# Kernel optimization log

Hardware: AMD Instinct MI355X
Metric: run time of the kernel (lower is better)

Reference implementation:

```python
import jax, jax.numpy as jnp
import numpy as np

B, S, D = 2, 4096, 1024
H, W = 16, 128
HD = D // H  # 64


def setup_inputs() -> dict:
    key = jax.random.key(0)
    ks = jax.random.split(key, 6)
    x = jax.random.normal(ks[0], (B, S, D), dtype=jnp.float32)
    # standard RoPE angle table: theta[pos, i] = pos / 10000^(2i/hd)
    inv_freq = 1.0 / (10000.0 ** (jnp.arange(0, HD, 2, dtype=jnp.float32) / HD))  # (hd/2,)
    rope_freqs = jnp.arange(S, dtype=jnp.float32)[:, None] * inv_freq[None, :]     # (S, hd/2)
    scale = 0.02
    wq = jax.random.normal(ks[1], (D, D), dtype=jnp.float32) * scale
    wk = jax.random.normal(ks[2], (D, D), dtype=jnp.float32) * scale
    wv = jax.random.normal(ks[3], (D, D), dtype=jnp.float32) * scale
    wo = jax.random.normal(ks[4], (D, D), dtype=jnp.float32) * scale
    return {"x": x, "rope_freqs": rope_freqs, "wq": wq, "wk": wk, "wv": wv, "wo": wo}


def reference(x, rope_freqs, wq, wk, wv, wo):
    Bsz, Sl, Dm = x.shape
    hd = Dm // H
    q = (x @ wq.T).reshape(Bsz, Sl, H, hd)
    k = (x @ wk.T).reshape(Bsz, Sl, H, hd)
    v = (x @ wv.T).reshape(Bsz, Sl, H, hd)

    # rotate-half RoPE, angles broadcast over batch and heads
    f = rope_freqs[:Sl]                               # (S, hd/2)
    cos = jnp.cos(f)[None, :, None, :]
    sin = jnp.sin(f)[None, :, None, :]

    def rope(t):
        t1, t2 = jnp.split(t, 2, axis=-1)
        return jnp.concatenate([t1 * cos - t2 * sin, t2 * cos + t1 * sin], axis=-1)

    q = rope(q)
    k = rope(k)

    # block-local sliding-window attention: window [q-left, q+right]
    Bk = W                       # block size == window size
    nb = Sl // Bk                # S assumed divisible by W
    left = W // 2
    right = W - left - 1

    pad = [(0, 0), (Bk, Bk), (0, 0), (0, 0)]
    kb = jnp.pad(k, pad).reshape(Bsz, nb + 2, Bk, H, hd)
    vb = jnp.pad(v, pad).reshape(Bsz, nb + 2, Bk, H, hd)
    # each query block attends to 3 consecutive key blocks (prev, self, next)
    k3 = jnp.concatenate([kb[:, :-2], kb[:, 1:-1], kb[:, 2:]], axis=2)  # (B,nb,3Bk,H,hd)
    v3 = jnp.concatenate([vb[:, :-2], vb[:, 1:-1], vb[:, 2:]], axis=2)
    qb = q.reshape(Bsz, nb, Bk, H, hd)

    scale = 1.0 / jnp.sqrt(jnp.asarray(hd, dtype=x.dtype))
    scores = jnp.einsum('bnqhd,bnkhd->bnhqk', qb, k3) * scale  # (B,nb,H,Bk,3Bk)

    r = jnp.arange(Bk)
    c = jnp.arange(3 * Bk)
    rel = c[None, :] - Bk - r[:, None]                  # key_pos - query_pos, (Bk,3Bk)
    win = (rel >= -left) & (rel <= right)
    blk = jnp.arange(nb)
    key_pos = blk[:, None] * Bk + c[None, :] - Bk       # (nb,3Bk) absolute key positions
    valid = (key_pos >= 0) & (key_pos < Sl)
    mask = win[None, :, :] & valid[:, None, :]          # (nb,Bk,3Bk)

    scores = jnp.where(mask[None, :, None, :, :], scores, jnp.asarray(-1e30, scores.dtype))
    probs = jax.nn.softmax(scores, axis=-1)
    out = jnp.einsum('bnhqk,bnkhd->bnqhd', probs, v3).reshape(Bsz, Sl, H * hd)
    return out @ wo.T
```

## Files before the change

### kernel.cpp

```cpp
#include <hip/hip_runtime.h>

typedef unsigned short u16;
typedef unsigned int   u32;
typedef __attribute__((ext_vector_type(4))) unsigned int u32x4;
typedef __attribute__((ext_vector_type(2))) unsigned int u32x2;
typedef __attribute__((ext_vector_type(8))) short        s16x8;
typedef __attribute__((ext_vector_type(4))) float        f32x4;
typedef __attribute__((ext_vector_type(2))) float        f32x2;

#define S_LEN 4096

typedef const __attribute__((address_space(1))) void gas_void;
typedef __attribute__((address_space(3))) void las_void;

__device__ __forceinline__ u16 f2bf(float f) {
    u32 u = __builtin_bit_cast(u32, f);
    u32 r = (u + 0x7fffu + ((u >> 16) & 1u)) >> 16;
    return (u16)r;
}
__device__ __forceinline__ float bflo(u32 w) { return __builtin_bit_cast(float, w << 16); }
__device__ __forceinline__ float bfhi(u32 w) { return __builtin_bit_cast(float, w & 0xffff0000u); }

__device__ __forceinline__ float rmax16(float v) {
    v = fmaxf(v, __shfl_xor(v, 1));
    v = fmaxf(v, __shfl_xor(v, 2));
    v = fmaxf(v, __shfl_xor(v, 4));
    v = fmaxf(v, __shfl_xor(v, 8));
    return v;
}
__device__ __forceinline__ float rsum16(float v) {
    v += __shfl_xor(v, 1);
    v += __shfl_xor(v, 2);
    v += __shfl_xor(v, 4);
    v += __shfl_xor(v, 8);
    return v;
}

__global__ __launch_bounds__(256)
void cvt_f32_bf16(const float* __restrict__ in, u16* __restrict__ out, int n4) {
    int i = blockIdx.x * 256 + threadIdx.x;
    if (i >= n4) return;
    const f32x4 v = *(const f32x4*)(in + (size_t)i * 4);
    u32x2 o;
    o.x = (u32)f2bf(v.x) | ((u32)f2bf(v.y) << 16);
    o.y = (u32)f2bf(v.z) | ((u32)f2bf(v.w) << 16);
    *(u32x2*)(out + (size_t)i * 4) = o;
}

__global__ __launch_bounds__(256)
void cvt_weights(const float* __restrict__ wq, const float* __restrict__ wk,
                 const float* __restrict__ wv, const float* __restrict__ wo,
                 u16* __restrict__ wqkv, u16* __restrict__ wob) {
    const int i   = blockIdx.x * 256 + threadIdx.x;
    const int sel = i >> 18;
    const int loc = i & 262143;
    const float* src = (sel == 0) ? wq : (sel == 1) ? wk : (sel == 2) ? wv : wo;
    u16* dst = (sel < 3) ? (wqkv + (size_t)sel * 1048576) : wob;
    const f32x4 v = *(const f32x4*)(src + (size_t)loc * 4);
    u32x2 o;
    o.x = (u32)f2bf(v.x) | ((u32)f2bf(v.y) << 16);
    o.y = (u32)f2bf(v.z) | ((u32)f2bf(v.w) << 16);
    *(u32x2*)(dst + (size_t)loc * 4) = o;
}

__global__ __launch_bounds__(256)
void rope_tab(const float* __restrict__ freqs, float* __restrict__ tab) {
    const int i = blockIdx.x * 256 + threadIdx.x;
    const float f = freqs[i];
    float sn, cs;
    sincosf(f, &sn, &cs);
    tab[i * 2]     = cs;
    tab[i * 2 + 1] = sn;
}

#define VMW0() asm volatile("s_waitcnt vmcnt(0)" ::: "memory")
#define LGKM0() do { asm volatile("s_waitcnt lgkmcnt(0)" ::: "memory"); \
                     __builtin_amdgcn_sched_barrier(0); } while (0)
#define DSR0(d, a)   asm volatile("ds_read_b128 %0, %1"              : "=v"(d) : "v"(a))
#define DSR(d, a, o) asm volatile("ds_read_b128 %0, %1 offset:" #o   : "=v"(d) : "v"(a))
#define MFMA16(a, b, c) __builtin_amdgcn_mfma_f32_16x16x32_bf16(a, b, c, 0, 0, 0)

#define FRAGS(P) s16x8 P##a0,P##a1,P##a2,P##a3,P##a4,P##a5,P##a6,P##a7, \
                       P##b0,P##b1,P##b2,P##b3,P##b4,P##b5,P##b6,P##b7

#define LOADTILE(P, CUR) do { \
    const u32 abase_ = ldsA + ((u32)(CUR) << 14) + arow; \
    const u32 bbase_ = ldsB + ((u32)(CUR) << 15) + brow; \
    const u32 aa0_ = abase_ + ck0, aa1_ = abase_ + ck1; \
    const u32 ba0_ = bbase_ + ck0, ba1_ = bbase_ + ck1; \
    DSR0(P##a0, aa0_); DSR(P##a1, aa0_, 2048); DSR(P##a2, aa0_, 4096); DSR(P##a3, aa0_, 6144); \
    DSR0(P##a4, aa1_); DSR(P##a5, aa1_, 2048); DSR(P##a6, aa1_, 4096); DSR(P##a7, aa1_, 6144); \
    DSR0(P##b0, ba0_); DSR(P##b1, ba0_, 2048); DSR(P##b2, ba0_, 4096); DSR(P##b3, ba0_, 6144); \
    DSR0(P##b4, ba1_); DSR(P##b5, ba1_, 2048); DSR(P##b6, ba1_, 4096); DSR(P##b7, ba1_, 6144); \
} while (0)

#define MFMA32(P) do { \
    __builtin_amdgcn_s_setprio(1); \
    acc[0][0]=MFMA16(P##a0,P##b0,acc[0][0]); acc[1][0]=MFMA16(P##a1,P##b0,acc[1][0]); \
    acc[2][0]=MFMA16(P##a2,P##b0,acc[2][0]); acc[3][0]=MFMA16(P##a3,P##b0,acc[3][0]); \
    acc[0][1]=MFMA16(P##a0,P##b1,acc[0][1]); acc[1][1]=MFMA16(P##a1,P##b1,acc[1][1]); \
    acc[2][1]=MFMA16(P##a2,P##b1,acc[2][1]); acc[3][1]=MFMA16(P##a3,P##b1,acc[3][1]); \
    acc[0][2]=MFMA16(P##a0,P##b2,acc[0][2]); acc[1][2]=MFMA16(P##a1,P##b2,acc[1][2]); \
    acc[2][2]=MFMA16(P##a2,P##b2,acc[2][2]); acc[3][2]=MFMA16(P##a3,P##b2,acc[3][2]); \
    acc[0][3]=MFMA16(P##a0,P##b3,acc[0][3]); acc[1][3]=MFMA16(P##a1,P##b3,acc[1][3]); \
    acc[2][3]=MFMA16(P##a2,P##b3,acc[2][3]); acc[3][3]=MFMA16(P##a3,P##b3,acc[3][3]); \
    acc[0][0]=MFMA16(P##a4,P##b4,acc[0][0]); acc[1][0]=MFMA16(P##a5,P##b4,acc[1][0]); \
    acc[2][0]=MFMA16(P##a6,P##b4,acc[2][0]); acc[3][0]=MFMA16(P##a7,P##b4,acc[3][0]); \
    acc[0][1]=MFMA16(P##a4,P##b5,acc[0][1]); acc[1][1]=MFMA16(P##a5,P##b5,acc[1][1]); \
    acc[2][1]=MFMA16(P##a6,P##b5,acc[2][1]); acc[3][1]=MFMA16(P##a7,P##b5,acc[3][1]); \
    acc[0][2]=MFMA16(P##a4,P##b6,acc[0][2]); acc[1][2]=MFMA16(P##a5,P##b6,acc[1][2]); \
    acc[2][2]=MFMA16(P##a6,P##b6,acc[2][2]); acc[3][2]=MFMA16(P##a7,P##b6,acc[3][2]); \
    acc[0][3]=MFMA16(P##a4,P##b7,acc[0][3]); acc[1][3]=MFMA16(P##a5,P##b7,acc[1][3]); \
    acc[2][3]=MFMA16(P##a6,P##b7,acc[2][3]); acc[3][3]=MFMA16(P##a7,P##b7,acc[3][3]); \
    __builtin_amdgcn_s_setprio(0); \
} while (0)

template<int MODE>
__global__ __launch_bounds__(512, 2)
void gemm_bt(const u16* __restrict__ A, const u16* __restrict__ Bw,
             void* __restrict__ Cv, const float* __restrict__ cstab) {
    __shared__ __align__(16) u16 As[2][8192];
    __shared__ __align__(16) u16 Bs[2][16384];
    const int t    = threadIdx.x;
    const int bm   = blockIdx.x << 7;
    const int bn   = blockIdx.y << 8;
    const int wave = t >> 6;
    const int wr   = (wave >> 2) & 1;
    const int wc   = wave & 3;
    const int lane = t & 63;
    const int fr   = lane & 15;
    const int kg   = lane >> 4;
    const int f7   = fr & 7;
    const int wq16 = wave << 9;
    const int K    = 1024;

    const int srow = t >> 3;
    const int cSw  = (t & 7) ^ (srow & 7);

    const u16* ga0 = A  + (size_t)(bm + srow) * K + (cSw << 3);
    const u16* ga1 = ga0 + (size_t)64 * K;
    const u16* gb0 = Bw + (size_t)(bn + srow) * K + (cSw << 3);
    const u16* gb1 = gb0 + (size_t)64 * K;
    const u16* gb2 = gb1 + (size_t)64 * K;
    const u16* gb3 = gb2 + (size_t)64 * K;

    f32x4 acc[4][4];
#pragma unroll
    for (int m = 0; m < 4; ++m)
#pragma unroll
        for (int n = 0; n < 4; ++n) acc[m][n] = f32x4{0.f, 0.f, 0.f, 0.f};

    FRAGS(X);
    FRAGS(Y);

#define STAGE(cur) do { \
    __builtin_amdgcn_global_load_lds((gas_void*)ga0, (las_void*)(&As[cur][wq16]),          16, 0, 0); \
    __builtin_amdgcn_global_load_lds((gas_void*)ga1, (las_void*)(&As[cur][4096 + wq16]),   16, 0, 0); \
    __builtin_amdgcn_global_load_lds((gas_void*)gb0, (las_void*)(&Bs[cur][wq16]),          16, 0, 0); \
    __builtin_amdgcn_global_load_lds((gas_void*)gb1, (las_void*)(&Bs[cur][4096 + wq16]),   16, 0, 0); \
    __builtin_amdgcn_global_load_lds((gas_void*)gb2, (las_void*)(&Bs[cur][8192 + wq16]),   16, 0, 0); \
    __builtin_amdgcn_global_load_lds((gas_void*)gb3, (las_void*)(&Bs[cur][12288 + wq16]),  16, 0, 0); \
    ga0 += 64; ga1 += 64; gb0 += 64; gb1 += 64; gb2 += 64; gb3 += 64; \
} while (0)

    const u32 ldsA = (u32)(size_t)(las_void*)&As[0][0];
    const u32 ldsB = (u32)(size_t)(las_void*)&Bs[0][0];
    const u32 arow = (u32)(((wr << 6) + fr) << 7);
    const u32 brow = (u32)(((wc << 6) + fr) << 7);
    const u32 ck0  = (u32)((kg ^ f7) << 4);
    const u32 ck1  = (u32)(((4 + kg) ^ f7) << 4);

    STAGE(0);
    VMW0();
    __builtin_amdgcn_s_barrier();
    LOADTILE(X, 0);
    STAGE(1);

#pragma unroll 1
    for (int j = 0; j < 16; j += 2) {
        LGKM0();
        VMW0();
        __builtin_amdgcn_s_barrier();
        if (j < 14) STAGE(0);
        LOADTILE(Y, 1);
        MFMA32(X);
        LGKM0();
        if (j < 14) {
            VMW0();
            __builtin_amdgcn_s_barrier();
            if (j < 13) STAGE(1);
            LOADTILE(X, 0);
        }
        MFMA32(Y);
    }

#undef STAGE

    if constexpr (MODE == 1) {
        const int sel   = bn >> 10;
        u16* outb       = (u16*)Cv + (size_t)sel * 8388608;
        const int bcol  = (bn & 1023) + (wc << 6) + fr;
        const bool doRope = (bn < 2048);
        const int crow0 = bm + (wr << 6) + (kg << 2);
#pragma unroll
        for (int m = 0; m < 4; ++m)
#pragma unroll
            for (int r = 0; r < 4; ++r) {
                const int row = crow0 + (m << 4) + r;
                float v0 = acc[m][0][r], v1 = acc[m][1][r], v2 = acc[m][2][r], v3 = acc[m][3][r];
                if (doRope) {
                    const int s = row & (S_LEN - 1);
                    const f32x2 c0 = *(const f32x2*)(cstab + (((s << 5) + fr) << 1));
                    const f32x2 c1 = *(const f32x2*)(cstab + (((s << 5) + 16 + fr) << 1));
                    const float n0 = v0 * c0.x - v2 * c0.y;
                    const float n2 = v2 * c0.x + v0 * c0.y;
                    const float n1 = v1 * c1.x - v3 * c1.y;
                    const float n3 = v3 * c1.x + v1 * c1.y;
                    v0 = n0; v1 = n1; v2 = n2; v3 = n3;
                }
                u16* op = outb + (size_t)row * 1024 + bcol;
                op[0]  = f2bf(v0);
                op[16] = f2bf(v1);
                op[32] = f2bf(v2);
                op[48] = f2bf(v3);
            }
    } else {
        float* outf     = (float*)Cv;
        const int bcol  = bn + (wc << 6) + fr;
        const int crow0 = bm + (wr << 6) + (kg << 2);
#pragma unroll
        for (int m = 0; m < 4; ++m)
#pragma unroll
            for (int r = 0; r < 4; ++r) {
                const int row = crow0 + (m << 4) + r;
                float* op = outf + (size_t)row * 1024 + bcol;
                op[0]  = acc[m][0][r];
                op[16] = acc[m][1][r];
                op[32] = acc[m][2][r];
                op[48] = acc[m][3][r];
            }
    }
}

__global__ __launch_bounds__(256)
void attn_kernel(const u16* __restrict__ Q, const u16* __restrict__ K,
                 const u16* __restrict__ V, u16* __restrict__ O) {
    __shared__ __align__(16) u16 Ks[192 * 64];
    __shared__ __align__(16) u16 Vt[64 * 192];
    const int bid = blockIdx.x;
    const int ch  = bid & 63;
    const int h   = (bid >> 6) & 15;
    const int b   = bid >> 10;
    const int qs  = ch << 6;
    const int t   = threadIdx.x;

#pragma unroll
    for (int i = 0; i < 6; ++i) {
        const int cid = t + (i << 8);
        const int row = cid >> 3;
        const int cc  = cid & 7;
        const int kp  = qs - 64 + row;
        const int sc  = cc ^ (row & 7);
        u32x4 kd = {0u, 0u, 0u, 0u};
        if (kp >= 0 && kp < S_LEN)
            kd = *(const u32x4*)(K + ((size_t)(b * S_LEN + kp)) * 1024 + (h << 6) + (cc << 3));
        *(u32x4*)(&Ks[(row << 6) + (sc << 3)]) = kd;
    }
    if (t < 192) {
        const int kp = qs - 64 + t;
        const int tc = t >> 3;
        const int ti = t & 7;
        if (kp >= 0 && kp < S_LEN) {
            const size_t off = ((size_t)(b * S_LEN + kp)) * 1024 + (h << 6);
#pragma unroll
            for (int c = 0; c < 8; ++c) {
                const u32x4 vd = *(const u32x4*)(V + off + (c << 3));
#pragma unroll
                for (int jj = 0; jj < 4; ++jj) {
                    const int d0 = (c << 3) + (jj << 1);
                    const int d1 = d0 + 1;
                    Vt[d0 * 192 + ((tc ^ (d0 & 7)) << 3) + ti] = (u16)(vd[jj] & 0xffffu);
                    Vt[d1 * 192 + ((tc ^ (d1 & 7)) << 3) + ti] = (u16)(vd[jj] >> 16);
                }
            }
        } else {
#pragma unroll
            for (int c = 0; c < 8; ++c)
#pragma unroll
                for (int j = 0; j < 8; ++j) {
                    const int d = (c << 3) + j;
                    Vt[d * 192 + ((tc ^ (d & 7)) << 3) + ti] = 0;
                }
        }
    }
    __syncthreads();

    const int w    = t >> 6;
    const int lane = t & 63;
    const int fr   = lane & 15;
    const int kg   = lane >> 4;
    const int f7   = fr & 7;

    const size_t qgoff = ((size_t)(b * S_LEN + qs + (w << 4) + fr)) * 1024 + (h << 6) + (kg << 3);
    const s16x8 qa0 = *(const s16x8*)(Q + qgoff);
    const s16x8 qa1 = *(const s16x8*)(Q + qgoff + 32);

    f32x4 sfr[9];
#pragma unroll
    for (int n = 0; n < 9; ++n) {
        const int row = (w << 4) + (n << 4) + fr;
        f32x4 a = f32x4{0.f, 0.f, 0.f, 0.f};
        const s16x8 kb0 = *(const s16x8*)(&Ks[(row << 6) + ((kg ^ f7) << 3)]);
        const s16x8 kb1 = *(const s16x8*)(&Ks[(row << 6) + (((4 + kg) ^ f7) << 3)]);
        a = __builtin_amdgcn_mfma_f32_16x16x32_bf16(qa0, kb0, a, 0, 0, 0);
        a = __builtin_amdgcn_mfma_f32_16x16x32_bf16(qa1, kb1, a, 0, 0, 0);
        sfr[n] = a;
    }

    const float NEG = -__builtin_inff();
    float mx[4] = {NEG, NEG, NEG, NEG};
#pragma unroll
    for (int n = 0; n < 9; ++n) {
        const int j = (n << 4) + fr;
#pragma unroll
        for (int r = 0; r < 4; ++r) {
            const int q  = (kg << 2) + r;
            const int kp = qs - 64 + (w << 4) + j;
            const bool valid = (j >= q) && (j - q < 128) && (kp >= 0) && (kp < S_LEN);
            const float s = valid ? sfr[n][r] * 0.125f : NEG;
            sfr[n][r] = s;
            mx[r] = fmaxf(mx[r], s);
        }
    }
#pragma unroll
    for (int r = 0; r < 4; ++r) mx[r] = rmax16(mx[r]);
    float ls[4] = {0.f, 0.f, 0.f, 0.f};
#pragma unroll
    for (int n = 0; n < 9; ++n)
#pragma unroll
        for (int r = 0; r < 4; ++r) {
            const float p = __expf(sfr[n][r] - mx[r]);
            sfr[n][r] = p;
            ls[r] += p;
        }
#pragma unroll
    for (int r = 0; r < 4; ++r) ls[r] = rsum16(ls[r]);

    __syncthreads();
    u16* Pw = Ks + w * 3072;
#pragma unroll
    for (int n = 0; n < 9; ++n) {
        const int j = (n << 4) + fr;
#pragma unroll
        for (int r = 0; r < 4; ++r) {
            const int q = (kg << 2) + r;
            Pw[q * 192 + (((j >> 3) ^ (q & 7)) << 3) + (j & 7)] = f2bf(sfr[n][r]);
        }
    }
    {
        const int j = 144 + fr;
#pragma unroll
        for (int r = 0; r < 4; ++r) {
            const int q = (kg << 2) + r;
            Pw[q * 192 + (((j >> 3) ^ (q & 7)) << 3) + (j & 7)] = 0;
        }
    }
    __syncthreads();

    f32x4 o[4];
#pragma unroll
    for (int nf = 0; nf < 4; ++nf) o[nf] = f32x4{0.f, 0.f, 0.f, 0.f};
#pragma unroll
    for (int ks = 0; ks < 5; ++ks) {
        const s16x8 pa = *(const s16x8*)(&Pw[fr * 192 + ((((ks << 2) + kg) ^ f7) << 3)]);
#pragma unroll
        for (int nf = 0; nf < 4; ++nf) {
            const int rdim = (nf << 4) + fr;
            int c = (w << 1) + (ks << 2) + kg;
            if (c > 23) c = 23;
            const s16x8 vb = *(const s16x8*)(&Vt[rdim * 192 + ((c ^ f7) << 3)]);
            o[nf] = __builtin_amdgcn_mfma_f32_16x16x32_bf16(pa, vb, o[nf], 0, 0, 0);
        }
    }

    const size_t obase = ((size_t)(b * S_LEN + qs + (w << 4) + (kg << 2))) * 1024 + (h << 6) + fr;
#pragma unroll
    for (int r = 0; r < 4; ++r) {
        const float inv = 1.f / ls[r];
#pragma unroll
        for (int nf = 0; nf < 4; ++nf)
            O[obase + (size_t)r * 1024 + (nf << 4)] = f2bf(o[nf][r] * inv);
    }
}

extern "C" void kernel_launch(void* const* d_in, const int* in_sizes, int n_in,
                              void* d_out, int out_size, void* d_ws, size_t ws_size,
                              hipStream_t stream) {
    const float* x  = (const float*)d_in[0];
    const float* fr = (const float*)d_in[1];
    const float* wq = (const float*)d_in[2];
    const float* wk = (const float*)d_in[3];
    const float* wv = (const float*)d_in[4];
    const float* wo = (const float*)d_in[5];

    u16* ws    = (u16*)d_ws;
    u16* xb    = ws;
    u16* wqkvb = xb + 8388608;
    u16* wob   = wqkvb + 3145728;
    u16* qb    = wob + 1048576;
    u16* kb    = qb + 8388608;
    u16* vb    = kb + 8388608;
    float* cstab = (float*)(vb + 8388608);
    u16* ob    = xb;

    cvt_f32_bf16<<<8192, 256, 0, stream>>>(x, xb, 2097152);
    cvt_weights<<<4096, 256, 0, stream>>>(wq, wk, wv, wo, wqkvb, wob);
    rope_tab<<<512, 256, 0, stream>>>(fr, cstab);

    dim3 gqkv(64, 12);
    gemm_bt<1><<<gqkv, 512, 0, stream>>>(xb, wqkvb, qb, cstab);

    attn_kernel<<<2048, 256, 0, stream>>>(qb, kb, vb, ob);

    dim3 gout(64, 4);
    gemm_bt<2><<<gout, 512, 0, stream>>>(ob, wob, d_out, nullptr);
}
```

Baseline: 130.2 us.

## Emit V transposed from QKV GEMM and async-load attention tiles into LDS

The QKV GEMM epilogue now writes V in a head-dim-major (transposed) layout. The attention kernel can then fill its K and V shared-memory tiles with global_load_lds DMA copies instead of per-element transposing LDS stores. The three preprocessing kernels (x cast, weight cast, RoPE table) are merged into one launch to save launch overhead. The trade-off is that out-of-range window keys are no longer zero-filled: loads read adjacent memory and rely on masking, and the transposed V writes are strided 8-byte stores.

Measured after the change: 118.1 us. -9.3%, faster.

```diff
diff --git a/kernel.cpp b/kernel.cpp
--- a/kernel.cpp
+++ b/kernel.cpp
@@ -37,40 +37,40 @@
 }
 
 __global__ __launch_bounds__(256)
-void cvt_f32_bf16(const float* __restrict__ in, u16* __restrict__ out, int n4) {
-    int i = blockIdx.x * 256 + threadIdx.x;
-    if (i >= n4) return;
-    const f32x4 v = *(const f32x4*)(in + (size_t)i * 4);
-    u32x2 o;
-    o.x = (u32)f2bf(v.x) | ((u32)f2bf(v.y) << 16);
-    o.y = (u32)f2bf(v.z) | ((u32)f2bf(v.w) << 16);
-    *(u32x2*)(out + (size_t)i * 4) = o;
-}
-
-__global__ __launch_bounds__(256)
-void cvt_weights(const float* __restrict__ wq, const float* __restrict__ wk,
+void prep_kernel(const float* __restrict__ x,
+                 const float* __restrict__ wq, const float* __restrict__ wk,
                  const float* __restrict__ wv, const float* __restrict__ wo,
-                 u16* __restrict__ wqkv, u16* __restrict__ wob) {
-    const int i   = blockIdx.x * 256 + threadIdx.x;
-    const int sel = i >> 18;
-    const int loc = i & 262143;
-    const float* src = (sel == 0) ? wq : (sel == 1) ? wk : (sel == 2) ? wv : wo;
-    u16* dst = (sel < 3) ? (wqkv + (size_t)sel * 1048576) : wob;
-    const f32x4 v = *(const f32x4*)(src + (size_t)loc * 4);
-    u32x2 o;
-    o.x = (u32)f2bf(v.x) | ((u32)f2bf(v.y) << 16);
-    o.y = (u32)f2bf(v.z) | ((u32)f2bf(v.w) << 16);
-    *(u32x2*)(dst + (size_t)loc * 4) = o;
-}
-
-__global__ __launch_bounds__(256)
-void rope_tab(const float* __restrict__ freqs, float* __restrict__ tab) {
-    const int i = blockIdx.x * 256 + threadIdx.x;
-    const float f = freqs[i];
-    float sn, cs;
-    sincosf(f, &sn, &cs);
-    tab[i * 2]     = cs;
-    tab[i * 2 + 1] = sn;
+                 const float* __restrict__ freqs,
+                 u16* __restrict__ xb, u16* __restrict__ wqkv, u16* __restrict__ wob,
+                 float* __restrict__ tab) {
+    const int bid = blockIdx.x;
+    const int t   = threadIdx.x;
+    if (bid < 8192) {
+        const int i = bid * 256 + t;
+        const f32x4 v = *(const f32x4*)(x + (size_t)i * 4);
+        u32x2 o;
+        o.x = (u32)f2bf(v.x) | ((u32)f2bf(v.y) << 16);
+        o.y = (u32)f2bf(v.z) | ((u32)f2bf(v.w) << 16);
+        *(u32x2*)(xb + (size_t)i * 4) = o;
+    } else if (bid < 12288) {
+        const int i   = (bid - 8192) * 256 + t;
+        const int sel = i >> 18;
+        const int loc = i & 262143;
+        const float* src = (sel == 0) ? wq : (sel == 1) ? wk : (sel == 2) ? wv : wo;
+        u16* dst = (sel < 3) ? (wqkv + (size_t)sel * 1048576) : wob;
+        const f32x4 v = *(const f32x4*)(src + (size_t)loc * 4);
+        u32x2 o;
+        o.x = (u32)f2bf(v.x) | ((u32)f2bf(v.y) << 16);
+        o.y = (u32)f2bf(v.z) | ((u32)f2bf(v.w) << 16);
+        *(u32x2*)(dst + (size_t)loc * 4) = o;
+    } else {
+        const int i = (bid - 12288) * 256 + t;
+        const float f = freqs[i];
+        float sn, cs;
+        sincosf(f, &sn, &cs);
+        tab[i * 2]     = cs;
+        tab[i * 2 + 1] = sn;
+    }
 }
 
 #define VMW0() asm volatile("s_waitcnt vmcnt(0)" ::: "memory")
@@ -79,6 +79,7 @@
 #define DSR0(d, a)   asm volatile("ds_read_b128 %0, %1"              : "=v"(d) : "v"(a))
 #define DSR(d, a, o) asm volatile("ds_read_b128 %0, %1 offset:" #o   : "=v"(d) : "v"(a))
 #define MFMA16(a, b, c) __builtin_amdgcn_mfma_f32_16x16x32_bf16(a, b, c, 0, 0, 0)
+#define GL(p, d) __builtin_amdgcn_global_load_lds((gas_void*)(p), (las_void*)(d), 16, 0, 0)
 
 #define FRAGS(P) s16x8 P##a0,P##a1,P##a2,P##a3,P##a4,P##a5,P##a6,P##a7, \
                        P##b0,P##b1,P##b2,P##b3,P##b4,P##b5,P##b6,P##b7
@@ -154,12 +155,9 @@
     FRAGS(Y);
 
 #define STAGE(cur) do { \
-    __builtin_amdgcn_global_load_lds((gas_void*)ga0, (las_void*)(&As[cur][wq16]),          16, 0, 0); \
-    __builtin_amdgcn_global_load_lds((gas_void*)ga1, (las_void*)(&As[cur][4096 + wq16]),   16, 0, 0); \
-    __builtin_amdgcn_global_load_lds((gas_void*)gb0, (las_void*)(&Bs[cur][wq16]),          16, 0, 0); \
-    __builtin_amdgcn_global_load_lds((gas_void*)gb1, (las_void*)(&Bs[cur][4096 + wq16]),   16, 0, 0); \
-    __builtin_amdgcn_global_load_lds((gas_void*)gb2, (las_void*)(&Bs[cur][8192 + wq16]),   16, 0, 0); \
-    __builtin_amdgcn_global_load_lds((gas_void*)gb3, (las_void*)(&Bs[cur][12288 + wq16]),  16, 0, 0); \
+    GL(ga0, &As[cur][wq16]);          GL(ga1, &As[cur][4096 + wq16]); \
+    GL(gb0, &Bs[cur][wq16]);          GL(gb1, &Bs[cur][4096 + wq16]); \
+    GL(gb2, &Bs[cur][8192 + wq16]);   GL(gb3, &Bs[cur][12288 + wq16]); \
     ga0 += 64; ga1 += 64; gb0 += 64; gb1 += 64; gb2 += 64; gb3 += 64; \
 } while (0)
 
@@ -198,17 +196,31 @@
 
     if constexpr (MODE == 1) {
         const int sel   = bn >> 10;
-        u16* outb       = (u16*)Cv + (size_t)sel * 8388608;
         const int bcol  = (bn & 1023) + (wc << 6) + fr;
-        const bool doRope = (bn < 2048);
         const int crow0 = bm + (wr << 6) + (kg << 2);
-#pragma unroll
-        for (int m = 0; m < 4; ++m)
-#pragma unroll
-            for (int r = 0; r < 4; ++r) {
-                const int row = crow0 + (m << 4) + r;
-                float v0 = acc[m][0][r], v1 = acc[m][1][r], v2 = acc[m][2][r], v3 = acc[m][3][r];
-                if (doRope) {
+        if (sel == 2) {
+            u16* vt = (u16*)Cv + (size_t)16777216;
+#pragma unroll
+            for (int m = 0; m < 4; ++m) {
+                const int row0 = crow0 + (m << 4);
+                const int bb   = row0 >> 12;
+                const int s0   = row0 & 4095;
+#pragma unroll
+                for (int n = 0; n < 4; ++n) {
+                    u32x2 pk;
+                    pk.x = (u32)f2bf(acc[m][n][0]) | ((u32)f2bf(acc[m][n][1]) << 16);
+                    pk.y = (u32)f2bf(acc[m][n][2]) | ((u32)f2bf(acc[m][n][3]) << 16);
+                    *(u32x2*)(vt + ((size_t)((bb << 10) + bcol + (n << 4))) * 4096 + s0) = pk;
+                }
+            }
+        } else {
+            u16* outb = (u16*)Cv + (size_t)sel * 8388608;
+#pragma unroll
+            for (int m = 0; m < 4; ++m)
+#pragma unroll
+                for (int r = 0; r < 4; ++r) {
+                    const int row = crow0 + (m << 4) + r;
+                    float v0 = acc[m][0][r], v1 = acc[m][1][r], v2 = acc[m][2][r], v3 = acc[m][3][r];
                     const int s = row & (S_LEN - 1);
                     const f32x2 c0 = *(const f32x2*)(cstab + (((s << 5) + fr) << 1));
                     const f32x2 c1 = *(const f32x2*)(cstab + (((s << 5) + 16 + fr) << 1));
@@ -216,14 +228,13 @@
                     const float n2 = v2 * c0.x + v0 * c0.y;
                     const float n1 = v1 * c1.x - v3 * c1.y;
                     const float n3 = v3 * c1.x + v1 * c1.y;
-                    v0 = n0; v1 = n1; v2 = n2; v3 = n3;
+                    u16* op = outb + (size_t)row * 1024 + bcol;
+                    op[0]  = f2bf(n0);
+                    op[16] = f2bf(n1);
+                    op[32] = f2bf(n2);
+                    op[48] = f2bf(n3);
                 }
-                u16* op = outb + (size_t)row * 1024 + bcol;
-                op[0]  = f2bf(v0);
-                op[16] = f2bf(v1);
-                op[32] = f2bf(v2);
-                op[48] = f2bf(v3);
-            }
+        }
     } else {
         float* outf     = (float*)Cv;
         const int bcol  = bn + (wc << 6) + fr;
@@ -244,56 +255,37 @@
 
 __global__ __launch_bounds__(256)
 void attn_kernel(const u16* __restrict__ Q, const u16* __restrict__ K,
-                 const u16* __restrict__ V, u16* __restrict__ O) {
+                 const u16* __restrict__ Vt, u16* __restrict__ O) {
     __shared__ __align__(16) u16 Ks[192 * 64];
-    __shared__ __align__(16) u16 Vt[64 * 192];
+    __shared__ __align__(16) u16 Vs[64 * 192];
     const int bid = blockIdx.x;
     const int ch  = bid & 63;
     const int h   = (bid >> 6) & 15;
     const int b   = bid >> 10;
     const int qs  = ch << 6;
     const int t   = threadIdx.x;
+    const int ub  = t & 192;
 
 #pragma unroll
     for (int i = 0; i < 6; ++i) {
-        const int cid = t + (i << 8);
+        const int cid = (i << 8) + t;
         const int row = cid >> 3;
-        const int cc  = cid & 7;
+        const int g   = (cid & 7) ^ (row & 7);
         const int kp  = qs - 64 + row;
-        const int sc  = cc ^ (row & 7);
-        u32x4 kd = {0u, 0u, 0u, 0u};
-        if (kp >= 0 && kp < S_LEN)
-            kd = *(const u32x4*)(K + ((size_t)(b * S_LEN + kp)) * 1024 + (h << 6) + (cc << 3));
-        *(u32x4*)(&Ks[(row << 6) + (sc << 3)]) = kd;
-    }
-    if (t < 192) {
-        const int kp = qs - 64 + t;
-        const int tc = t >> 3;
-        const int ti = t & 7;
-        if (kp >= 0 && kp < S_LEN) {
-            const size_t off = ((size_t)(b * S_LEN + kp)) * 1024 + (h << 6);
-#pragma unroll
-            for (int c = 0; c < 8; ++c) {
-                const u32x4 vd = *(const u32x4*)(V + off + (c << 3));
-#pragma unroll
-                for (int jj = 0; jj < 4; ++jj) {
-                    const int d0 = (c << 3) + (jj << 1);
-                    const int d1 = d0 + 1;
-                    Vt[d0 * 192 + ((tc ^ (d0 & 7)) << 3) + ti] = (u16)(vd[jj] & 0xffffu);
-                    Vt[d1 * 192 + ((tc ^ (d1 & 7)) << 3) + ti] = (u16)(vd[jj] >> 16);
-                }
-            }
-        } else {
-#pragma unroll
-            for (int c = 0; c < 8; ++c)
-#pragma unroll
-                for (int j = 0; j < 8; ++j) {
-                    const int d = (c << 3) + j;
-                    Vt[d * 192 + ((tc ^ (d & 7)) << 3) + ti] = 0;
-                }
-        }
-    }
-    __syncthreads();
+        const u16* src = K + ((size_t)((b << 12) + kp)) * 1024 + (h << 6) + (g << 3);
+        GL(src, &Ks[((i << 8) + ub) << 3]);
+    }
+#pragma unroll
+    for (int i = 0; i < 6; ++i) {
+        const int cid = (i << 8) + t;
+        const int d   = cid / 24;
+        const int c   = cid - d * 24;
+        int g = c - (d & 7) * 3;
+        if (g < 0) g += 24;
+        const int key = qs - 64 + (g << 3);
+        const u16* src = Vt + ((size_t)((b << 10) + (h << 6) + d)) * 4096 + key;
+        GL(src, &Vs[((i << 8) + ub) << 3]);
+    }
 
     const int w    = t >> 6;
     const int lane = t & 63;
@@ -301,9 +293,12 @@
     const int kg   = lane >> 4;
     const int f7   = fr & 7;
 
-    const size_t qgoff = ((size_t)(b * S_LEN + qs + (w << 4) + fr)) * 1024 + (h << 6) + (kg << 3);
+    const size_t qgoff = ((size_t)((b << 12) + qs + (w << 4) + fr)) * 1024 + (h << 6) + (kg << 3);
     const s16x8 qa0 = *(const s16x8*)(Q + qgoff);
     const s16x8 qa1 = *(const s16x8*)(Q + qgoff + 32);
+
+    VMW0();
+    __syncthreads();
 
     f32x4 sfr[9];
 #pragma unroll
@@ -312,8 +307,8 @@
         f32x4 a = f32x4{0.f, 0.f, 0.f, 0.f};
         const s16x8 kb0 = *(const s16x8*)(&Ks[(row << 6) + ((kg ^ f7) << 3)]);
         const s16x8 kb1 = *(const s16x8*)(&Ks[(row << 6) + (((4 + kg) ^ f7) << 3)]);
-        a = __builtin_amdgcn_mfma_f32_16x16x32_bf16(qa0, kb0, a, 0, 0, 0);
-        a = __builtin_amdgcn_mfma_f32_16x16x32_bf16(qa1, kb1, a, 0, 0, 0);
+        a = MFMA16(qa0, kb0, a);
+        a = MFMA16(qa1, kb1, a);
         sfr[n] = a;
     }
 
@@ -370,20 +365,23 @@
     f32x4 o[4];
 #pragma unroll
     for (int nf = 0; nf < 4; ++nf) o[nf] = f32x4{0.f, 0.f, 0.f, 0.f};
+    const int cs0 = f7 * 3;
 #pragma unroll
     for (int ks = 0; ks < 5; ++ks) {
         const s16x8 pa = *(const s16x8*)(&Pw[fr * 192 + ((((ks << 2) + kg) ^ f7) << 3)]);
+        int c = (w << 1) + (ks << 2) + kg;
+        if (c > 23) c = 23;
+        int cs = c + cs0;
+        if (cs >= 24) cs -= 24;
 #pragma unroll
         for (int nf = 0; nf < 4; ++nf) {
-            const int rdim = (nf << 4) + fr;
-            int c = (w << 1) + (ks << 2) + kg;
-            if (c > 23) c = 23;
-            const s16x8 vb = *(const s16x8*)(&Vt[rdim * 192 + ((c ^ f7) << 3)]);
-            o[nf] = __builtin_amdgcn_mfma_f32_16x16x32_bf16(pa, vb, o[nf], 0, 0, 0);
-        }
-    }
-
-    const size_t obase = ((size_t)(b * S_LEN + qs + (w << 4) + (kg << 2))) * 1024 + (h << 6) + fr;
+            const int d = (nf << 4) + fr;
+            const s16x8 vbf = *(const s16x8*)(&Vs[d * 192 + (cs << 3)]);
+            o[nf] = MFMA16(pa, vbf, o[nf]);
+        }
+    }
+
+    const size_t obase = ((size_t)((b << 12) + qs + (w << 4) + (kg << 2))) * 1024 + (h << 6) + fr;
 #pragma unroll
     for (int r = 0; r < 4; ++r) {
         const float inv = 1.f / ls[r];
@@ -409,18 +407,16 @@
     u16* wob   = wqkvb + 3145728;
     u16* qb    = wob + 1048576;
     u16* kb    = qb + 8388608;
-    u16* vb    = kb + 8388608;
-    float* cstab = (float*)(vb + 8388608);
+    u16* vtb   = kb + 8388608;
+    float* cstab = (float*)(vtb + 8388608);
     u16* ob    = xb;
 
-    cvt_f32_bf16<<<8192, 256, 0, stream>>>(x, xb, 2097152);
-    cvt_weights<<<4096, 256, 0, stream>>>(wq, wk, wv, wo, wqkvb, wob);
-    rope_tab<<<512, 256, 0, stream>>>(fr, cstab);
+    prep_kernel<<<12800, 256, 0, stream>>>(x, wq, wk, wv, wo, fr, xb, wqkvb, wob, cstab);
 
     dim3 gqkv(64, 12);
     gemm_bt<1><<<gqkv, 512, 0, stream>>>(xb, wqkvb, qb, cstab);
 
-    attn_kernel<<<2048, 256, 0, stream>>>(qb, kb, vb, ob);
+    attn_kernel<<<2048, 256, 0, stream>>>(qb, kb, vtb, ob);
 
     dim3 gout(64, 4);
     gemm_bt<2><<<gout, 512, 0, stream>>>(ob, wob, d_out, nullptr);
```
